# Kernel optimization log

Hardware: AMD Instinct MI355X
Metric: run time of the kernel (lower is better)

## Reference

```python
import jax, jax.numpy as jnp
import numpy as np

B, NQ, NK, D, H = 4, 2048, 2048, 1024, 16
HD = D // H


def setup_inputs() -> dict:
    key = jax.random.key(0)
    ks = jax.random.split(key, 11)
    s = 1.0 / np.sqrt(D)
    return {
        "q": jax.random.normal(ks[0], (B, NQ, D), jnp.float32),
        "k": jax.random.normal(ks[1], (B, NK, D), jnp.float32),
        "v": jax.random.normal(ks[2], (B, NK, D), jnp.float32),
        "Wq": jax.random.uniform(ks[3], (D, D), jnp.float32, -s, s),
        "bq": jax.random.uniform(ks[4], (D,), jnp.float32, -s, s),
        "Wk": jax.random.uniform(ks[5], (D, D), jnp.float32, -s, s),
        "bk": jax.random.uniform(ks[6], (D,), jnp.float32, -s, s),
        "Wv": jax.random.uniform(ks[7], (D, D), jnp.float32, -s, s),
        "bv": jax.random.uniform(ks[8], (D,), jnp.float32, -s, s),
        "Wo": jax.random.uniform(ks[9], (D, D), jnp.float32, -s, s),
        "bo": jax.random.uniform(ks[10], (D,), jnp.float32, -s, s),
    }


def reference(q, k, v, Wq, bq, Wk, bk, Wv, bv, Wo, bo):
    # Linear projections (torch Linear: x @ W.T + b), split into heads [B,H,N,HD]
    qh = (q @ Wq.T + bq).reshape(B, NQ, H, HD).transpose(0, 2, 1, 3)
    kh = (k @ Wk.T + bk).reshape(B, NK, H, HD).transpose(0, 2, 1, 3)
    vh = (v @ Wv.T + bv).reshape(B, NK, H, HD).transpose(0, 2, 1, 3)
    scores = jnp.einsum('bhqd,bhkd->bhqk', qh, kh) / np.sqrt(HD)  # [B,H,Nq,Nk]
    probs = jax.nn.softmax(scores, axis=-1)
    out = jnp.einsum('bhqk,bhkd->bhqd', probs, vh)
    out = out.transpose(0, 2, 1, 3).reshape(B, NQ, D)
    return out @ Wo.T + bo
```

## Files before the change

kernel.cpp:

```cpp
#include <hip/hip_runtime.h>
#include <hip/hip_bf16.h>
#include <cstdint>
#include <cstddef>


typedef __bf16 bf16x8 __attribute__((ext_vector_type(8)));
typedef float f32x4 __attribute__((ext_vector_type(4)));

#define BB 4
#define NQ 2048
#define NK 2048
#define DD 1024
#define HH 16
#define HD 64

#define QSCALE (0.125f * 1.4426950408889634f)

#if __has_builtin(__builtin_amdgcn_exp2f)
#define EXP2F(x) __builtin_amdgcn_exp2f(x)
#else
#define EXP2F(x) exp2f(x)
#endif

__device__ inline void gld_lds16(const void* g, void* lds) {
  __builtin_amdgcn_global_load_lds(
      (__attribute__((address_space(1))) unsigned int*)(g),
      (__attribute__((address_space(3))) unsigned int*)(lds),
      16, 0, 0);
}

__device__ inline bool probe_f32(const void* p) {
  const unsigned short* u = (const unsigned short*)p;
  int bad = 0;
#pragma unroll
  for (int i = 0; i < 64; ++i) {
    const int e = (u[2 * i] >> 7) & 0xFF;
    bad += (e > 0x8F) ? 1 : 0;
  }
  return bad >= 4;
}

__device__ inline bf16x8 cvt8(const float* src) {
  union { bf16x8 v; __hip_bfloat16 h[8]; } u;
#pragma unroll
  for (int j = 0; j < 8; ++j) u.h[j] = __float2bfloat16(src[j]);
  return u.v;
}

__global__ __launch_bounds__(256) void cvt_all(
    const void* __restrict__ q, const void* __restrict__ k,
    const void* __restrict__ v,
    const void* __restrict__ Wq, const void* __restrict__ Wk,
    const void* __restrict__ Wv, const void* __restrict__ Wo,
    __hip_bfloat16* __restrict__ qb, __hip_bfloat16* __restrict__ kb,
    __hip_bfloat16* __restrict__ vb, __hip_bfloat16* __restrict__ Wb) {
  const int bidx = blockIdx.x;
  const void* src; __hip_bfloat16* dst; size_t voff;
  if (bidx < 1536) {
    const int s = bidx >> 9;
    src = s == 0 ? q : (s == 1 ? k : v);
    dst = s == 0 ? qb : (s == 1 ? kb : vb);
    voff = (size_t)(bidx & 511) * 2048;
  } else {
    const int wi = (bidx - 1536) >> 6;
    src = wi == 0 ? Wq : (wi == 1 ? Wk : (wi == 2 ? Wv : Wo));
    dst = Wb + (size_t)wi * (DD * DD);
    voff = (size_t)((bidx - 1536) & 63) * 2048;
  }
  __shared__ int sflag;
  if (threadIdx.x == 0) sflag = probe_f32(src) ? 1 : 0;
  __syncthreads();
  const bool f32 = sflag != 0;
  const int t = threadIdx.x;
#pragma unroll
  for (int i = 0; i < 8; ++i) {
    const size_t j = voff + (size_t)i * 256 + t;
    if (f32) {
      union { f32x4 v2[2]; float f[8]; } u;
      const f32x4* s4 = (const f32x4*)src;
      u.v2[0] = s4[j * 2]; u.v2[1] = s4[j * 2 + 1];
      *(bf16x8*)(dst + j * 8) = cvt8(u.f);
    } else {
      *(f32x4*)(dst + j * 8) = ((const f32x4*)src)[j];
    }
  }
}

__global__ __launch_bounds__(256, 3) void gemm_fast(
    const __hip_bfloat16* __restrict__ qb, const __hip_bfloat16* __restrict__ kb,
    const __hip_bfloat16* __restrict__ vb, const __hip_bfloat16* __restrict__ At,
    const __hip_bfloat16* __restrict__ Wb,
    const void* __restrict__ bq, const void* __restrict__ bk,
    const void* __restrict__ bv, const void* __restrict__ bo,
    const void* __restrict__ WoOrig,
    void* __restrict__ Qp, void* __restrict__ Kp,
    void* __restrict__ Vt, void* __restrict__ Out, int cfg0) {
  __shared__ __align__(16) __hip_bfloat16 sA[128 * 64];
  __shared__ __align__(16) __hip_bfloat16 sB[128 * 64];
  const int t = threadIdx.x;
  const int wave = t >> 6, lane = t & 63;
  const int q4 = lane >> 4, c16 = lane & 15;
  const int xr = c16 & 7;
  const int wr = wave >> 1, wc = wave & 1;

  const int bid = blockIdx.x;
  const int xcd = bid & 7, idx = bid >> 3;
  const int z = idx >> 6;
  const int r6 = idx & 63;
  const int bm = xcd * 8 + (r6 >> 3);
  const int bn = r6 & 7;
  const int cfg = cfg0 + z;

  const __hip_bfloat16* A; const void* biasv; void* Cv; int mode; float scale = 1.f;
  if (cfg == 0)      { A = qb; biasv = bq; Cv = Qp; mode = 0; scale = QSCALE; }
  else if (cfg == 1) { A = kb; biasv = bk; Cv = Kp; mode = 0; }
  else if (cfg == 2) { A = vb; biasv = bv; Cv = Vt; mode = 1; }
  else               { A = At; biasv = bo; Cv = Out; mode = 2; }
  const __hip_bfloat16* Bm = Wb + (size_t)cfg * (DD * DD);

  const bool bias_f32 = probe_f32(biasv);
  const bool c_f32 = (mode == 2) && probe_f32(WoOrig);

  f32x4 acc[4][4];
#pragma unroll
  for (int i = 0; i < 4; ++i)
#pragma unroll
    for (int j = 0; j < 4; ++j) acc[i][j] = (f32x4){0.f, 0.f, 0.f, 0.f};

  const size_t baseA = (size_t)bm * 128 * DD;
  const size_t baseB = (size_t)bn * 128 * DD;

  size_t offA[4], offB[4];
  int lslot[4];
#pragma unroll
  for (int i = 0; i < 4; ++i) {
    const int slot = i * 256 + t;
    const int row = slot >> 3, pg = (slot & 7) ^ (row & 7);
    lslot[i] = slot;
    offA[i] = baseA + (size_t)row * DD + pg * 8;
    offB[i] = baseB + (size_t)row * DD + pg * 8;
  }

  for (int k0 = 0; k0 < DD; k0 += 64) {
    __syncthreads();
#pragma unroll
    for (int i = 0; i < 4; ++i)
      gld_lds16(A + offA[i] + k0, sA + lslot[i] * 8);
#pragma unroll
    for (int i = 0; i < 4; ++i)
      gld_lds16(Bm + offB[i] + k0, sB + lslot[i] * 8);
    __syncthreads();

#pragma unroll
    for (int ks = 0; ks < 2; ++ks) {
      bf16x8 af[4], bfm[4];
#pragma unroll
      for (int rt = 0; rt < 4; ++rt)
        af[rt] = *(const bf16x8*)(sA + (wr * 64 + rt * 16 + c16) * 64 +
                                  ((ks * 4 + q4) ^ xr) * 8);
#pragma unroll
      for (int ct = 0; ct < 4; ++ct)
        bfm[ct] = *(const bf16x8*)(sB + (wc * 64 + ct * 16 + c16) * 64 +
                                   ((ks * 4 + q4) ^ xr) * 8);
#pragma unroll
      for (int rt = 0; rt < 4; ++rt)
#pragma unroll
        for (int ct = 0; ct < 4; ++ct)
          acc[rt][ct] = __builtin_amdgcn_mfma_f32_16x16x32_bf16(af[rt], bfm[ct],
                                                                acc[rt][ct], 0, 0, 0);
    }
  }

  if (mode == 1) {
    __syncthreads();
    __hip_bfloat16* sT = wc ? sB : sA;
#pragma unroll
    for (int ct = 0; ct < 4; ++ct) {
      const int col = ct * 16 + c16;
      const int colg = bn * 128 + wc * 64 + col;
      const float bvx = bias_f32 ? ((const float*)biasv)[colg]
                                 : __bfloat162float(((const __hip_bfloat16*)biasv)[colg]);
      const int sw = (col & 7) << 3;
#pragma unroll
      for (int rt = 0; rt < 4; ++rt) {
        union { uint2 u; __hip_bfloat16 hx[4]; } pk;
#pragma unroll
        for (int r = 0; r < 4; ++r)
          pk.hx[r] = __float2bfloat16((acc[rt][ct][r] + bvx) * scale);
        const int rowl = wr * 64 + rt * 16 + q4 * 4;
        *(uint2*)(sT + col * 128 + (rowl ^ sw)) = pk.u;
      }
    }
    __syncthreads();
    const int bb = bm >> 4;
    const int kb0 = (bm & 15) * 128;
#pragma unroll
    for (int i = 0; i < 8; ++i) {
      const int idx2 = i * 256 + t;
      const int half = idx2 >> 10;
      const int rem = idx2 & 1023;
      const int col = rem >> 4;
      const int kc = rem & 15;
      const __hip_bfloat16* sTh = half ? sB : sA;
      bf16x8 vv = *(const bf16x8*)(sTh + col * 128 + ((kc * 8) ^ ((col & 7) << 3)));
      const int hh = bn * 2 + half;
      *(bf16x8*)((__hip_bfloat16*)Cv +
                 (size_t)((bb * HH + hh) * HD + col) * NK + kb0 + kc * 8) = vv;
    }
    return;
  }

  const int row0 = bm * 128 + wr * 64 + q4 * 4;
  const int col0 = bn * 128 + wc * 64 + c16;
#pragma unroll
  for (int ct = 0; ct < 4; ++ct) {
    const int col = col0 + ct * 16;
    const float bvx = bias_f32 ? ((const float*)biasv)[col]
                               : __bfloat162float(((const __hip_bfloat16*)biasv)[col]);
#pragma unroll
    for (int rt = 0; rt < 4; ++rt) {
#pragma unroll
      for (int r = 0; r < 4; ++r) {
        const int row = row0 + rt * 16 + r;
        const float val = (acc[rt][ct][r] + bvx) * scale;
        if (c_f32) {
          ((float*)Cv)[(size_t)row * DD + col] = val;
        } else {
          ((__hip_bfloat16*)Cv)[(size_t)row * DD + col] = __float2bfloat16(val);
        }
      }
    }
  }
}

__device__ inline void ld_slot(bool f32, const void* basep, size_t eoff,
                               f32x4& lo, f32x4& hi) {
  if (f32) {
    const f32x4* p = (const f32x4*)((const float*)basep + eoff);
    lo = p[0]; hi = p[1];
  } else {
    lo = *(const f32x4*)((const __hip_bfloat16*)basep + eoff);
  }
}

__device__ inline void st_slot(bool f32, __hip_bfloat16* dst, f32x4 lo, f32x4 hi) {
  if (f32) {
    union { f32x4 v[2]; float f[8]; } u;
    u.v[0] = lo; u.v[1] = hi;
    *(bf16x8*)dst = cvt8(u.f);
  } else {
    *(f32x4*)dst = lo;
  }
}

__global__ __launch_bounds__(256, 3) void gemm_mha(
    const void* __restrict__ qin, const void* __restrict__ kin,
    const void* __restrict__ vin, const void* __restrict__ ain,
    const void* __restrict__ Wq, const void* __restrict__ bq,
    const void* __restrict__ Wk, const void* __restrict__ bk,
    const void* __restrict__ Wv, const void* __restrict__ bv,
    const void* __restrict__ Wo, const void* __restrict__ bo,
    void* __restrict__ Qp, void* __restrict__ Kp,
    void* __restrict__ Vt, void* __restrict__ Out, int cfg0) {
  __shared__ __align__(16) __hip_bfloat16 sA[2][128 * 32];
  __shared__ __align__(16) __hip_bfloat16 sB[2][128 * 32];
  const int t = threadIdx.x;
  const int wave = t >> 6, lane = t & 63;
  const int q4 = lane >> 4, c16 = lane & 15;
  const int wr = wave >> 1, wc = wave & 1;

  const int bid = blockIdx.x;
  const int xcd = bid & 7, idx = bid >> 3;
  const int z = idx >> 6;
  const int r6 = idx & 63;
  const int bm = xcd * 8 + (r6 >> 3);
  const int bn = r6 & 7;
  const int cfg = cfg0 + z;

  const void *Av, *Bv, *biasv; void* Cv; int mode; float scale = 1.f;
  if (cfg == 0)      { Av = qin; Bv = Wq; biasv = bq; Cv = Qp; mode = 0; scale = QSCALE; }
  else if (cfg == 1) { Av = kin; Bv = Wk; biasv = bk; Cv = Kp; mode = 0; }
  else if (cfg == 2) { Av = vin; Bv = Wv; biasv = bv; Cv = Vt; mode = 1; }
  else               { Av = ain; Bv = Wo; biasv = bo; Cv = Out; mode = 2; }

  const bool a_f32 = probe_f32(Av);
  const bool b_f32 = probe_f32(Bv);
  const bool c_f32 = (mode == 2) && b_f32;

  f32x4 acc[4][4];
#pragma unroll
  for (int i = 0; i < 4; ++i)
#pragma unroll
    for (int j = 0; j < 4; ++j) acc[i][j] = (f32x4){0.f, 0.f, 0.f, 0.f};

  const size_t baseA = (size_t)bm * 128 * DD;
  const size_t baseB = (size_t)bn * 128 * DD;
  const int po = ((q4) ^ (c16 & 3)) * 8;

  size_t offA[2], offB[2];
  int lslot[2];
#pragma unroll
  for (int i = 0; i < 2; ++i) {
    const int slot = i * 256 + t;
    const int row = slot >> 2, pg = (slot & 3) ^ (row & 3);
    lslot[i] = slot;
    offA[i] = baseA + (size_t)row * DD + pg * 8;
    offB[i] = baseB + (size_t)row * DD + pg * 8;
  }

  f32x4 Alo[2], Ahi[2], Blo[2], Bhi[2];
#pragma unroll
  for (int i = 0; i < 2; ++i) {
    ld_slot(a_f32, Av, offA[i], Alo[i], Ahi[i]);
    ld_slot(b_f32, Bv, offB[i], Blo[i], Bhi[i]);
  }

  for (int k0 = 0, it = 0; k0 < DD; k0 += 32, ++it) {
    const int p = it & 1;
#pragma unroll
    for (int i = 0; i < 2; ++i) {
      st_slot(a_f32, &sA[p][lslot[i] * 8], Alo[i], Ahi[i]);
      st_slot(b_f32, &sB[p][lslot[i] * 8], Blo[i], Bhi[i]);
    }
    __syncthreads();

    if (k0 + 32 < DD) {
#pragma unroll
      for (int i = 0; i < 2; ++i) {
        ld_slot(a_f32, Av, offA[i] + k0 + 32, Alo[i], Ahi[i]);
        ld_slot(b_f32, Bv, offB[i] + k0 + 32, Blo[i], Bhi[i]);
      }
    }

    bf16x8 af[4], bfm[4];
#pragma unroll
    for (int rt = 0; rt < 4; ++rt)
      af[rt] = *(const bf16x8*)(&sA[p][0] + (wr * 64 + rt * 16 + c16) * 32 + po);
#pragma unroll
    for (int ct = 0; ct < 4; ++ct)
      bfm[ct] = *(const bf16x8*)(&sB[p][0] + (wc * 64 + ct * 16 + c16) * 32 + po);
#pragma unroll
    for (int rt = 0; rt < 4; ++rt)
#pragma unroll
      for (int ct = 0; ct < 4; ++ct)
        acc[rt][ct] = __builtin_amdgcn_mfma_f32_16x16x32_bf16(af[rt], bfm[ct],
                                                              acc[rt][ct], 0, 0, 0);
  }

  const int row0 = bm * 128 + wr * 64 + q4 * 4;
  const int col0 = bn * 128 + wc * 64 + c16;
#pragma unroll
  for (int ct = 0; ct < 4; ++ct) {
    const int col = col0 + ct * 16;
    const float bvx = b_f32 ? ((const float*)biasv)[col]
                            : __bfloat162float(((const __hip_bfloat16*)biasv)[col]);
#pragma unroll
    for (int rt = 0; rt < 4; ++rt) {
#pragma unroll
      for (int r = 0; r < 4; ++r) {
        const int row = row0 + rt * 16 + r;
        const float val = (acc[rt][ct][r] + bvx) * scale;
        if (mode == 1) {
          const int b = row >> 11, key = row & 2047;
          const int h = col >> 6, hd = col & 63;
          ((__hip_bfloat16*)Cv)[(size_t)((b * HH + h) * HD + hd) * NK + key] =
              __float2bfloat16(val);
        } else if (c_f32) {
          ((float*)Cv)[(size_t)row * DD + col] = val;
        } else {
          ((__hip_bfloat16*)Cv)[(size_t)row * DD + col] = __float2bfloat16(val);
        }
      }
    }
  }
}

__global__ __launch_bounds__(256, 4) void flash_attn(
    const __hip_bfloat16* Qp, const __hip_bfloat16* __restrict__ Kp,
    const __hip_bfloat16* __restrict__ Vt, __hip_bfloat16* Ao) {
  __shared__ __align__(16) __hip_bfloat16 sQP[128 * 64];
  __shared__ __align__(16) __hip_bfloat16 sK[2][64 * 64];
  __shared__ __align__(16) __hip_bfloat16 sV[64 * 64];

  const int t = threadIdx.x;
  const int wave = t >> 6, lane = t & 63;
  const int q4 = lane >> 4, c16 = lane & 15;
  const int xr = c16 & 7;

  const int bid = blockIdx.x;
  const int xcd = bid & 7, idx = bid >> 3;
  const int bh = xcd * 8 + (idx >> 4);
  const int qt = idx & 15;
  const int b = bh >> 4, h = bh & 15;

#pragma unroll
  for (int i = 0; i < 4; ++i) {
    const int slot = i * 256 + t;
    const int row = slot >> 3, pg = (slot & 7) ^ (row & 7);
    gld_lds16(Qp + ((size_t)(b * NQ + qt * 128 + row) * DD + h * 64 + pg * 8),
              sQP + slot * 8);
  }
#pragma unroll
  for (int i = 0; i < 2; ++i) {
    const int slot = i * 256 + t;
    const int row = slot >> 3, pg = (slot & 7) ^ (row & 7);
    gld_lds16(Kp + ((size_t)(b * NK + row) * DD + h * 64 + pg * 8),
              &sK[0][0] + slot * 8);
  }

  f32x4 o[2][4];
#pragma unroll
  for (int g = 0; g < 2; ++g)
#pragma unroll
    for (int i = 0; i < 4; ++i) o[g][i] = (f32x4){0.f, 0.f, 0.f, 0.f};
  float lp0 = 0.f, lp1 = 0.f;

  __syncthreads();

  bf16x8 aq[2][2];
#pragma unroll
  for (int qg = 0; qg < 2; ++qg)
#pragma unroll
    for (int ks = 0; ks < 2; ++ks)
      aq[qg][ks] = *(const bf16x8*)(sQP + (wave * 32 + qg * 16 + c16) * 64 +
                                    ((ks * 4 + q4) ^ xr) * 8);

  const int prow0 = wave * 32 + c16;
  const int prow1 = wave * 32 + 16 + c16;

  for (int kt = 0; kt < NK / 64; ++kt) {
    const int p = kt & 1;
#pragma unroll
    for (int i = 0; i < 2; ++i) {
      const int slot = i * 256 + t;
      const int row = slot >> 3, pg = (slot & 7) ^ (row & 7);
      gld_lds16(Vt + ((size_t)(bh * 64 + row) * NK + kt * 64 + pg * 8),
                &sV[0] + slot * 8);
    }
    if (kt + 1 < NK / 64) {
#pragma unroll
      for (int i = 0; i < 2; ++i) {
        const int slot = i * 256 + t;
        const int row = slot >> 3, pg = (slot & 7) ^ (row & 7);
        gld_lds16(Kp + ((size_t)(b * NK + (kt + 1) * 64 + row) * DD + h * 64 + pg * 8),
                  &sK[p ^ 1][0] + slot * 8);
      }
    }

    f32x4 s[2][4];
#pragma unroll
    for (int ct = 0; ct < 4; ++ct) {
      bf16x8 bk0 = *(const bf16x8*)(&sK[p][0] + (ct * 16 + c16) * 64 + ((0 + q4) ^ xr) * 8);
      bf16x8 bk1 = *(const bf16x8*)(&sK[p][0] + (ct * 16 + c16) * 64 + ((4 + q4) ^ xr) * 8);
#pragma unroll
      for (int qg = 0; qg < 2; ++qg) {
        f32x4 z = (f32x4){0.f, 0.f, 0.f, 0.f};
        z = __builtin_amdgcn_mfma_f32_16x16x32_bf16(bk0, aq[qg][0], z, 0, 0, 0);
        z = __builtin_amdgcn_mfma_f32_16x16x32_bf16(bk1, aq[qg][1], z, 0, 0, 0);
        s[qg][ct] = z;
      }
    }

#pragma unroll
    for (int qg = 0; qg < 2; ++qg) {
      const int prow = qg ? prow1 : prow0;
#pragma unroll
      for (int ct = 0; ct < 4; ++ct) {
        union { uint2 u; __hip_bfloat16 hx[4]; } pk;
#pragma unroll
        for (int r = 0; r < 4; ++r) {
          const float pe = EXP2F(s[qg][ct][r]);
          if (qg) lp1 += pe; else lp0 += pe;
          pk.hx[r] = __float2bfloat16(pe);
        }
        const int pc = (ct * 2 + (q4 >> 1)) ^ xr;
        *(uint2*)(sQP + prow * 64 + pc * 8 + (q4 & 1) * 4) = pk.u;
      }
    }

    __syncthreads();

#pragma unroll
    for (int kk = 0; kk < 2; ++kk) {
      bf16x8 bvf[4];
#pragma unroll
      for (int ct2 = 0; ct2 < 4; ++ct2)
        bvf[ct2] = *(const bf16x8*)(&sV[0] + (ct2 * 16 + c16) * 64 + ((kk * 4 + q4) ^ xr) * 8);
      bf16x8 ap0 = *(const bf16x8*)(sQP + prow0 * 64 + ((kk * 4 + q4) ^ xr) * 8);
      bf16x8 ap1 = *(const bf16x8*)(sQP + prow1 * 64 + ((kk * 4 + q4) ^ xr) * 8);
#pragma unroll
      for (int ct2 = 0; ct2 < 4; ++ct2) {
        o[0][ct2] = __builtin_amdgcn_mfma_f32_16x16x32_bf16(ap0, bvf[ct2], o[0][ct2], 0, 0, 0);
        o[1][ct2] = __builtin_amdgcn_mfma_f32_16x16x32_bf16(ap1, bvf[ct2], o[1][ct2], 0, 0, 0);
      }
    }

    __syncthreads();
  }

  float lr[2][4];
#pragma unroll
  for (int qg = 0; qg < 2; ++qg) {
    float lq = (qg ? lp1 : lp0);
    lq += __shfl_xor(lq, 16, 64);
    lq += __shfl_xor(lq, 32, 64);
    const float linv = 1.f / lq;
#pragma unroll
    for (int r = 0; r < 4; ++r) lr[qg][r] = __shfl(linv, q4 * 4 + r, 64);
  }

#pragma unroll
  for (int qg = 0; qg < 2; ++qg)
#pragma unroll
    for (int ct2 = 0; ct2 < 4; ++ct2)
#pragma unroll
      for (int r = 0; r < 4; ++r) {
        const size_t row = (size_t)(b * NQ + qt * 128 + wave * 32 + qg * 16 + q4 * 4 + r);
        Ao[row * DD + h * 64 + ct2 * 16 + c16] = __float2bfloat16(o[qg][ct2][r] * lr[qg][r]);
      }
}

extern "C" void kernel_launch(void* const* d_in, const int* in_sizes, int n_in,
                              void* d_out, int out_size, void* d_ws, size_t ws_size,
                              hipStream_t stream) {
  const void* q  = d_in[0];
  const void* k  = d_in[1];
  const void* v  = d_in[2];
  const void* Wq = d_in[3];
  const void* bq = d_in[4];
  const void* Wk = d_in[5];
  const void* bk = d_in[6];
  const void* Wv = d_in[7];
  const void* bv = d_in[8];
  const void* Wo = d_in[9];
  const void* bo = d_in[10];

  const size_t MP = (size_t)BB * NQ;
  const size_t MAT = MP * DD;
  __hip_bfloat16* Qp = (__hip_bfloat16*)d_ws;
  __hip_bfloat16* Vt = Qp + MAT;
  __hip_bfloat16* Kp = (__hip_bfloat16*)d_out;
  __hip_bfloat16* At = Qp;

  const size_t NEED = (4 * MAT + 4 * (size_t)(DD * DD)) * sizeof(__hip_bfloat16);
  if (ws_size >= NEED) {
    __hip_bfloat16* kb = Vt + MAT;
    __hip_bfloat16* vb = kb + MAT;
    __hip_bfloat16* Wb = vb + MAT;
    __hip_bfloat16* qb = (__hip_bfloat16*)d_out + MAT;

    cvt_all<<<dim3(1792), 256, 0, stream>>>(q, k, v, Wq, Wk, Wv, Wo,
                                            qb, kb, vb, Wb);
    gemm_fast<<<dim3(1536), 256, 0, stream>>>(qb, kb, vb, At, Wb,
                                              bq, bk, bv, bo, Wo,
                                              Qp, Kp, Vt, d_out, 0);
    flash_attn<<<dim3(1024), 256, 0, stream>>>(Qp, Kp, Vt, At);
    gemm_fast<<<dim3(512), 256, 0, stream>>>(qb, kb, vb, At, Wb,
                                             bq, bk, bv, bo, Wo,
                                             Qp, Kp, Vt, d_out, 3);
  } else {
    gemm_mha<<<dim3(1536), 256, 0, stream>>>(
        q, k, v, At, Wq, bq, Wk, bk, Wv, bv, Wo, bo, Qp, Kp, Vt, d_out, 0);
    flash_attn<<<dim3(1024), 256, 0, stream>>>(Qp, Kp, Vt, At);
    gemm_mha<<<dim3(512), 256, 0, stream>>>(
        q, k, v, At, Wq, bq, Wk, bk, Wv, bv, Wo, bo, Qp, Kp, Vt, d_out, 3);
  }
}
```

Measured before the change: 338.9 us.

## Compute softmax row sums via MFMA with ones vector, add setprio, raise occupancy

Replaces the per-element scalar accumulation of softmax denominators with an extra MFMA per k-step that multiplies the bf16 probability tile by a vector of ones. This removes the scalar adds and the cross-lane shuffles at the end. It also wraps the MFMA phases in s_setprio and raises the minimum-blocks hint on gemm_fast from 3 to 4. Summing the bf16-rounded probabilities keeps the denominator consistent with the numerator, but it adds MFMA work and may put register pressure on the GEMM kernel.

```diff
diff --git a/kernel.cpp b/kernel.cpp
--- a/kernel.cpp
+++ b/kernel.cpp
@@ -86,7 +86,7 @@
   }
 }
 
-__global__ __launch_bounds__(256, 3) void gemm_fast(
+__global__ __launch_bounds__(256, 4) void gemm_fast(
     const __hip_bfloat16* __restrict__ qb, const __hip_bfloat16* __restrict__ kb,
     const __hip_bfloat16* __restrict__ vb, const __hip_bfloat16* __restrict__ At,
     const __hip_bfloat16* __restrict__ Wb,
@@ -413,7 +413,13 @@
   for (int g = 0; g < 2; ++g)
 #pragma unroll
     for (int i = 0; i < 4; ++i) o[g][i] = (f32x4){0.f, 0.f, 0.f, 0.f};
-  float lp0 = 0.f, lp1 = 0.f;
+  f32x4 lacc[2];
+  lacc[0] = (f32x4){0.f, 0.f, 0.f, 0.f};
+  lacc[1] = (f32x4){0.f, 0.f, 0.f, 0.f};
+
+  union { bf16x8 v; unsigned short u[8]; } one8;
+#pragma unroll
+  for (int j = 0; j < 8; ++j) one8.u[j] = 0x3F80;
 
   __syncthreads();
 
@@ -448,6 +454,7 @@
     }
 
     f32x4 s[2][4];
+    __builtin_amdgcn_s_setprio(1);
 #pragma unroll
     for (int ct = 0; ct < 4; ++ct) {
       bf16x8 bk0 = *(const bf16x8*)(&sK[p][0] + (ct * 16 + c16) * 64 + ((0 + q4) ^ xr) * 8);
@@ -460,6 +467,7 @@
         s[qg][ct] = z;
       }
     }
+    __builtin_amdgcn_s_setprio(0);
 
 #pragma unroll
     for (int qg = 0; qg < 2; ++qg) {
@@ -468,11 +476,8 @@
       for (int ct = 0; ct < 4; ++ct) {
         union { uint2 u; __hip_bfloat16 hx[4]; } pk;
 #pragma unroll
-        for (int r = 0; r < 4; ++r) {
-          const float pe = EXP2F(s[qg][ct][r]);
-          if (qg) lp1 += pe; else lp0 += pe;
-          pk.hx[r] = __float2bfloat16(pe);
-        }
+        for (int r = 0; r < 4; ++r)
+          pk.hx[r] = __float2bfloat16(EXP2F(s[qg][ct][r]));
         const int pc = (ct * 2 + (q4 >> 1)) ^ xr;
         *(uint2*)(sQP + prow * 64 + pc * 8 + (q4 & 1) * 4) = pk.u;
       }
@@ -480,6 +485,7 @@
 
     __syncthreads();
 
+    __builtin_amdgcn_s_setprio(1);
 #pragma unroll
     for (int kk = 0; kk < 2; ++kk) {
       bf16x8 bvf[4];
@@ -488,26 +494,24 @@
         bvf[ct2] = *(const bf16x8*)(&sV[0] + (ct2 * 16 + c16) * 64 + ((kk * 4 + q4) ^ xr) * 8);
       bf16x8 ap0 = *(const bf16x8*)(sQP + prow0 * 64 + ((kk * 4 + q4) ^ xr) * 8);
       bf16x8 ap1 = *(const bf16x8*)(sQP + prow1 * 64 + ((kk * 4 + q4) ^ xr) * 8);
+      lacc[0] = __builtin_amdgcn_mfma_f32_16x16x32_bf16(ap0, one8.v, lacc[0], 0, 0, 0);
+      lacc[1] = __builtin_amdgcn_mfma_f32_16x16x32_bf16(ap1, one8.v, lacc[1], 0, 0, 0);
 #pragma unroll
       for (int ct2 = 0; ct2 < 4; ++ct2) {
         o[0][ct2] = __builtin_amdgcn_mfma_f32_16x16x32_bf16(ap0, bvf[ct2], o[0][ct2], 0, 0, 0);
         o[1][ct2] = __builtin_amdgcn_mfma_f32_16x16x32_bf16(ap1, bvf[ct2], o[1][ct2], 0, 0, 0);
       }
     }
-
-    __syncthreads();
-  }
-
-  float lr[2][4];
-#pragma unroll
-  for (int qg = 0; qg < 2; ++qg) {
-    float lq = (qg ? lp1 : lp0);
-    lq += __shfl_xor(lq, 16, 64);
-    lq += __shfl_xor(lq, 32, 64);
-    const float linv = 1.f / lq;
-#pragma unroll
-    for (int r = 0; r < 4; ++r) lr[qg][r] = __shfl(linv, q4 * 4 + r, 64);
-  }
+    __builtin_amdgcn_s_setprio(0);
+
+    __syncthreads();
+  }
+
+  float linv[2][4];
+#pragma unroll
+  for (int qg = 0; qg < 2; ++qg)
+#pragma unroll
+    for (int r = 0; r < 4; ++r) linv[qg][r] = 1.f / lacc[qg][r];
 
 #pragma unroll
   for (int qg = 0; qg < 2; ++qg)
@@ -516,7 +520,7 @@
 #pragma unroll
       for (int r = 0; r < 4; ++r) {
         const size_t row = (size_t)(b * NQ + qt * 128 + wave * 32 + qg * 16 + q4 * 4 + r);
-        Ao[row * DD + h * 64 + ct2 * 16 + c16] = __float2bfloat16(o[qg][ct2][r] * lr[qg][r]);
+        Ao[row * DD + h * 64 + ct2 * 16 + c16] = __float2bfloat16(o[qg][ct2][r] * linv[qg][r]);
       }
 }
 
```

After: 393.9 us. +16.2%, slower.
